# Optimization experiments

Measured on AMD Instinct MI355X. Metric: run time of the kernel, lower is better.

## Reference

```python
import jax, jax.numpy as jnp
import numpy as np
from jax import lax

RADIUS = 4
SIGMA_1 = 5.0
SIGMA_2 = 1.0


def _gaussian_kernel_3d(radius, sigma):
    x = np.linspace(-radius, radius, 2 * radius + 1)
    xx, yy, zz = np.meshgrid(x, x, x)
    dist2 = xx ** 2 + yy ** 2 + zz ** 2
    k = np.exp(-dist2 / (2.0 * sigma ** 2)).astype(np.float32)
    return jnp.asarray(k)[None, None]  # [O=1, I=1, D, H, W]


def _conv3d_same(x, kernel, radius):
    # x: [B,1,D,H,W], kernel: [1,1,kd,kh,kw]
    pad = [(radius, radius)] * 3
    return lax.conv_general_dilated(
        x, kernel, window_strides=(1, 1, 1), padding=pad,
        dimension_numbers=('NCDHW', 'OIDHW', 'NCDHW'))


def setup_inputs() -> dict:
    key = jax.random.key(0)
    k1, k2 = jax.random.split(key)
    labels = jax.random.uniform(k1, (4, 1, 160, 160, 160), dtype=jnp.float32)
    inputs = jax.random.uniform(k2, (4, 1, 160, 160, 160), dtype=jnp.float32)
    return {"labels": labels, "inputs": inputs}


def reference(labels, inputs):
    kernel = _gaussian_kernel_3d(RADIUS, SIGMA_1)
    num_classes = 2
    p0 = labels[:, 0:1]  # [B,1,D,H,W]
    loss = jnp.float32(0.0)
    for k in range(num_classes):
        class_probs = p0 if k == 0 else 1.0 - p0
        class_mean = (jnp.mean(inputs * class_probs, axis=(2, 3, 4), keepdims=True)
                      / (jnp.mean(class_probs, axis=(2, 3, 4), keepdims=True) + 1e-5))
        diff = jnp.sum((inputs - class_mean) ** 2, axis=1, keepdims=True)  # [B,1,D,H,W]
        weights = jnp.exp(-(diff ** 2) / (SIGMA_2 ** 2))
        numerator = jnp.sum(class_probs * _conv3d_same(class_probs * weights, kernel, RADIUS))
        denominator = jnp.sum(class_probs * _conv3d_same(weights, kernel, RADIUS))
        # L1Loss(scalar, 0) == abs(scalar)
        loss = loss + jnp.abs(numerator / (denominator + 1e-6))
    return jnp.float32(num_classes) - loss
```

## Files before the change

### kernel.cpp

```cpp
#include <hip/hip_runtime.h>
#include <math.h>

#define NX   160
#define N2   25600
#define N3   4096000
#define NB   4

#define NTILES_XY 16000
#define TILES_PER_B 4000
#define NBLK_Z 800

#define SA_W 52
#define SB_W 36

__device__ __constant__ float G1[9] = {
    0.72614903f, 0.83527021f, 0.92311635f, 0.98019867f, 1.0f,
    0.98019867f, 0.92311635f, 0.83527021f, 0.72614903f};

#define ES_FULL 7.92946852f
__device__ __constant__ float ES_M[4] = {3.46473426f, 2.48453559f, 1.56141924f,
                                         0.72614903f};
__device__ inline float edge_sum(int i) {
    float s = ES_FULL;
    if (i < 4) s -= ES_M[i];
    if (i > NX - 5) s -= ES_M[NX - 1 - i];
    return s;
}

__device__ inline float4 f4_zero() { return make_float4(0.f, 0.f, 0.f, 0.f); }
__device__ inline float4 f4_axpy(float a, float4 b, float4 c) {
    return make_float4(c.x + a * b.x, c.y + a * b.y, c.z + a * b.z, c.w + a * b.w);
}

template <int NV>
__device__ inline void block_reduce_store(double* vals, double* dst) {
    __shared__ double red[4][NV];
    int lane = threadIdx.x & 63;
    int wave = threadIdx.x >> 6;
#pragma unroll
    for (int v = 0; v < NV; ++v) {
        double x = vals[v];
#pragma unroll
        for (int off = 32; off > 0; off >>= 1) x += __shfl_down(x, off, 64);
        if (lane == 0) red[wave][v] = x;
    }
    __syncthreads();
    if (threadIdx.x < NV) {
        int v = threadIdx.x;
        dst[v] = red[0][v] + red[1][v] + red[2][v] + red[3][v];
    }
}

__global__ __launch_bounds__(256) void conv_xy_kernel(
    const float* __restrict__ labels, const float* __restrict__ inputs,
    float* __restrict__ t, double* __restrict__ pS) {
    __shared__ float sA[40 * SA_W];
    __shared__ float sB[40 * SB_W];

    int bid = blockIdx.x;
    int tileX = bid % 5;
    int tileY = (bid / 5) % 5;
    int zb = bid / 25;
    int sliceOff = zb * N2;
    int x0 = tileX * 32, y0 = tileY * 32;
    int tid = threadIdx.x;

    for (int i = tid; i < 480; i += 256) {
        int row = i / 12, c = i % 12;
        int gx = x0 - 8 + 4 * c;
        int gy = y0 - 4 + row;
        float4 v = f4_zero();
        if (gy >= 0 && gy < NX && gx >= 0 && gx <= NX - 4)
            v = *(const float4*)&labels[sliceOff + gy * NX + gx];
        *(float4*)&sA[row * SA_W + 4 * c] = v;
    }
    __syncthreads();

    for (int i = tid; i < 320; i += 256) {
        int r = i >> 3, x4 = i & 7;
        const float* row = &sA[r * SA_W + 4 * x4];
        float4 a = *(const float4*)&row[4];
        float4 b = *(const float4*)&row[8];
        float4 c = *(const float4*)&row[12];
        float w[12] = {a.x, a.y, a.z, a.w, b.x, b.y, b.z, b.w,
                       c.x, c.y, c.z, c.w};
        float4 o = f4_zero();
#pragma unroll
        for (int d = 0; d < 9; ++d) {
            float g = G1[d];
            o.x += g * w[d];
            o.y += g * w[d + 1];
            o.z += g * w[d + 2];
            o.w += g * w[d + 3];
        }
        *(float4*)&sB[r * SB_W + 4 * x4] = o;
    }
    __syncthreads();

    int oy = tid >> 3, x4 = tid & 7;
    float4 acc = f4_zero();
#pragma unroll
    for (int d = 0; d < 9; ++d) {
        float4 v = *(const float4*)&sB[(oy + d) * SB_W + 4 * x4];
        acc = f4_axpy(G1[d], v, acc);
    }
    int gi = sliceOff + (y0 + oy) * NX + (x0 + 4 * x4);
    *(float4*)&t[gi] = acc;

    float4 p = *(const float4*)&sA[(oy + 4) * SA_W + 4 * x4 + 8];
    float4 in = *(const float4*)&inputs[gi];
    float sp = p.x + p.y + p.z + p.w;
    float sip = in.x * p.x + in.y * p.y + in.z * p.z + in.w * p.w;
    float si = in.x + in.y + in.z + in.w;
    double vals[3] = {(double)sp, (double)sip, (double)si};
    block_reduce_store<3>(vals, pS + 3 * bid);
}

__global__ __launch_bounds__(256) void reduce_S_kernel(
    const double* __restrict__ pS, double* __restrict__ S) {
    int b = blockIdx.x;
    double v0 = 0, v1 = 0, v2 = 0;
    for (int i = threadIdx.x; i < TILES_PER_B; i += 256) {
        const double* p = pS + 3 * (b * TILES_PER_B + i);
        v0 += p[0]; v1 += p[1]; v2 += p[2];
    }
    double vals[3] = {v0, v1, v2};
    block_reduce_store<3>(vals, S + 3 * b);
}

__global__ __launch_bounds__(256) void conv_z_reduce_kernel(
    const float* __restrict__ t, const float* __restrict__ labels,
    const float* __restrict__ inputs, const double* __restrict__ S,
    double* __restrict__ pZ) {
    int tidg = blockIdx.x * 256 + threadIdx.x;
    int x4 = tidg % 40;
    int r = tidg / 40;
    int y = r % NX;
    r /= NX;
    int zc = r % 8;
    int b = r / 8;

    double sp = S[3 * b + 0], sip = S[3 * b + 1], si = S[3 * b + 2];
    const double Nv = (double)N3;
    float m0 = (float)((sip / Nv) / (sp / Nv + 1e-5));
    float m1 = (float)(((si - sip) / Nv) / ((Nv - sp) / Nv + 1e-5));

    int x = x4 * 4;
    float ey = edge_sum(y);
    float cx[4] = {edge_sum(x) * ey, edge_sum(x + 1) * ey,
                   edge_sum(x + 2) * ey, edge_sum(x + 3) * ey};

    int z0 = zc * 20;
    int base = b * N3 + y * NX + x;

    float4 win[9];
#pragma unroll
    for (int d = 0; d < 9; ++d) {
        int z = z0 - 4 + d;
        win[d] = (z >= 0 && z < NX) ? *(const float4*)&t[base + z * N2]
                                    : f4_zero();
    }

    float n0 = 0.f, d0 = 0.f, n1 = 0.f, d1 = 0.f;
    for (int zb = 0; zb < 5; ++zb) {
        int z = z0 + 4 * zb;
        float4 tn[4], pv[4], iv[4];
#pragma unroll
        for (int j = 0; j < 4; ++j) {
            int zl = z + j + 5;
            tn[j] = (zl < NX) ? *(const float4*)&t[base + zl * N2] : f4_zero();
            int gi = base + (z + j) * N2;
            pv[j] = *(const float4*)&labels[gi];
            iv[j] = *(const float4*)&inputs[gi];
        }
#pragma unroll
        for (int j = 0; j < 4; ++j) {
            float4 c4 = f4_zero();
#pragma unroll
            for (int d = 0; d < 9; ++d) c4 = f4_axpy(G1[d], win[d], c4);
            float ez = edge_sum(z + j);
            float pc[4] = {pv[j].x, pv[j].y, pv[j].z, pv[j].w};
            float ic[4] = {iv[j].x, iv[j].y, iv[j].z, iv[j].w};
            float cc[4] = {c4.x, c4.y, c4.z, c4.w};
#pragma unroll
            for (int l = 0; l < 4; ++l) {
                float c1 = cx[l] * ez - cc[l];
                float df0 = ic[l] - m0; df0 *= df0;
                float w0 = __expf(-df0 * df0);
                float df1 = ic[l] - m1; df1 *= df1;
                float w1 = __expf(-df1 * df1);
                n0 += cc[l] * pc[l] * w0;
                d0 += cc[l] * w0;
                n1 += c1 * (1.f - pc[l]) * w1;
                d1 += c1 * w1;
            }
#pragma unroll
            for (int d = 0; d < 8; ++d) win[d] = win[d + 1];
            win[8] = tn[j];
        }
    }
    double vals[4] = {(double)n0, (double)d0, (double)n1, (double)d1};
    block_reduce_store<4>(vals, pZ + 4 * blockIdx.x);
}

__global__ __launch_bounds__(256) void finalize_kernel(
    const double* __restrict__ pZ, float* __restrict__ out) {
    double a0 = 0, a1 = 0, a2 = 0, a3 = 0;
    for (int i = threadIdx.x; i < NBLK_Z; i += 256) {
        const double* p = pZ + 4 * i;
        a0 += p[0]; a1 += p[1]; a2 += p[2]; a3 += p[3];
    }
    __shared__ double red[4][4];
    int lane = threadIdx.x & 63;
    int wave = threadIdx.x >> 6;
    double vals[4] = {a0, a1, a2, a3};
#pragma unroll
    for (int v = 0; v < 4; ++v) {
        double x = vals[v];
#pragma unroll
        for (int off = 32; off > 0; off >>= 1) x += __shfl_down(x, off, 64);
        if (lane == 0) red[wave][v] = x;
    }
    __syncthreads();
    if (threadIdx.x == 0) {
        double acc[4];
#pragma unroll
        for (int v = 0; v < 4; ++v)
            acc[v] = red[0][v] + red[1][v] + red[2][v] + red[3][v];
        double r0 = fabs(acc[0] / (acc[1] + 1e-6));
        double r1 = fabs(acc[2] / (acc[3] + 1e-6));
        out[0] = (float)(2.0 - r0 - r1);
    }
}

extern "C" void kernel_launch(void* const* d_in, const int* in_sizes, int n_in,
                              void* d_out, int out_size, void* d_ws, size_t ws_size,
                              hipStream_t stream) {
    const float* labels = (const float*)d_in[0];
    const float* inputs = (const float*)d_in[1];
    float* out = (float*)d_out;

    double* pS = (double*)d_ws;
    double* S  = (double*)((char*)d_ws + 384000);
    double* pZ = (double*)((char*)d_ws + 384096);
    float*  t  = (float*)((char*)d_ws + 524288);

    hipLaunchKernelGGL(conv_xy_kernel, dim3(NTILES_XY), dim3(256), 0, stream,
                       labels, inputs, t, pS);
    hipLaunchKernelGGL(reduce_S_kernel, dim3(NB), dim3(256), 0, stream, pS, S);
    hipLaunchKernelGGL(conv_z_reduce_kernel, dim3(NBLK_Z), dim3(256), 0, stream,
                       t, labels, inputs, S, pZ);
    hipLaunchKernelGGL(finalize_kernel, dim3(1), dim3(256), 0, stream, pZ, out);
}
```

Measured before the change: 206.4 us.

## Fuse XY and Z convolution passes per slab, dropping intermediate volume

Removes the global intermediate XY-convolved volume. Each block now recomputes the XY convolution of labels plane by plane in shared memory and streams the results through a 9-deep Z register window over a 10-plane slab. Global sums move into a separate streaming reduction kernel. This avoids writing and re-reading a 65MB intermediate, at the cost of recomputing 8 halo planes per slab (about 1.8x XY work) and many more syncthreads.

```diff
diff --git a/kernel.cpp b/kernel.cpp
--- a/kernel.cpp
+++ b/kernel.cpp
@@ -6,9 +6,10 @@
 #define N3   4096000
 #define NB   4
 
-#define NTILES_XY 16000
-#define TILES_PER_B 4000
-#define NBLK_Z 800
+#define Z_SLAB 10
+#define NBLK_F 1600
+#define NBLK_S 1000
+#define SBLK_PER_B 250
 
 #define SA_W 52
 #define SB_W 36
@@ -51,34 +52,23 @@
     }
 }
 
-__global__ __launch_bounds__(256) void conv_xy_kernel(
-    const float* __restrict__ labels, const float* __restrict__ inputs,
-    float* __restrict__ t, double* __restrict__ pS) {
-    __shared__ float sA[40 * SA_W];
-    __shared__ float sB[40 * SB_W];
-
-    int bid = blockIdx.x;
-    int tileX = bid % 5;
-    int tileY = (bid / 5) % 5;
-    int zb = bid / 25;
-    int sliceOff = zb * N2;
-    int x0 = tileX * 32, y0 = tileY * 32;
-    int tid = threadIdx.x;
-
+__device__ inline float4 t_plane(const float* __restrict__ labels,
+                                 float* sA, float* sB, int planeOff,
+                                 int x0, int y0, int tid, int oy, int x4) {
     for (int i = tid; i < 480; i += 256) {
         int row = i / 12, c = i % 12;
         int gx = x0 - 8 + 4 * c;
         int gy = y0 - 4 + row;
         float4 v = f4_zero();
         if (gy >= 0 && gy < NX && gx >= 0 && gx <= NX - 4)
-            v = *(const float4*)&labels[sliceOff + gy * NX + gx];
+            v = *(const float4*)&labels[planeOff + gy * NX + gx];
         *(float4*)&sA[row * SA_W + 4 * c] = v;
     }
     __syncthreads();
 
     for (int i = tid; i < 320; i += 256) {
-        int r = i >> 3, x4 = i & 7;
-        const float* row = &sA[r * SA_W + 4 * x4];
+        int r = i >> 3, xx = i & 7;
+        const float* row = &sA[r * SA_W + 4 * xx];
         float4 a = *(const float4*)&row[4];
         float4 b = *(const float4*)&row[8];
         float4 c = *(const float4*)&row[12];
@@ -93,25 +83,37 @@
             o.z += g * w[d + 2];
             o.w += g * w[d + 3];
         }
-        *(float4*)&sB[r * SB_W + 4 * x4] = o;
-    }
-    __syncthreads();
-
-    int oy = tid >> 3, x4 = tid & 7;
+        *(float4*)&sB[r * SB_W + 4 * xx] = o;
+    }
+    __syncthreads();
+
     float4 acc = f4_zero();
 #pragma unroll
     for (int d = 0; d < 9; ++d) {
         float4 v = *(const float4*)&sB[(oy + d) * SB_W + 4 * x4];
         acc = f4_axpy(G1[d], v, acc);
     }
-    int gi = sliceOff + (y0 + oy) * NX + (x0 + 4 * x4);
-    *(float4*)&t[gi] = acc;
-
-    float4 p = *(const float4*)&sA[(oy + 4) * SA_W + 4 * x4 + 8];
-    float4 in = *(const float4*)&inputs[gi];
-    float sp = p.x + p.y + p.z + p.w;
-    float sip = in.x * p.x + in.y * p.y + in.z * p.z + in.w * p.w;
-    float si = in.x + in.y + in.z + in.w;
+    return acc;
+}
+
+__global__ __launch_bounds__(256) void sums_kernel(
+    const float* __restrict__ labels, const float* __restrict__ inputs,
+    double* __restrict__ pS) {
+    int bid = blockIdx.x, tid = threadIdx.x;
+    int b = bid / SBLK_PER_B;
+    int blk = bid % SBLK_PER_B;
+    int base = b * N3;
+    float sp = 0.f, sip = 0.f, si = 0.f;
+#pragma unroll 4
+    for (int k = 0; k < 16; ++k) {
+        int f4i = blk * 256 + tid + k * 64000;
+        int gi = base + 4 * f4i;
+        float4 p = *(const float4*)&labels[gi];
+        float4 in = *(const float4*)&inputs[gi];
+        sp += p.x + p.y + p.z + p.w;
+        sip += in.x * p.x + in.y * p.y + in.z * p.z + in.w * p.w;
+        si += in.x + in.y + in.z + in.w;
+    }
     double vals[3] = {(double)sp, (double)sip, (double)si};
     block_reduce_store<3>(vals, pS + 3 * bid);
 }
@@ -120,94 +122,95 @@
     const double* __restrict__ pS, double* __restrict__ S) {
     int b = blockIdx.x;
     double v0 = 0, v1 = 0, v2 = 0;
-    for (int i = threadIdx.x; i < TILES_PER_B; i += 256) {
-        const double* p = pS + 3 * (b * TILES_PER_B + i);
+    for (int i = threadIdx.x; i < SBLK_PER_B; i += 256) {
+        const double* p = pS + 3 * (b * SBLK_PER_B + i);
         v0 += p[0]; v1 += p[1]; v2 += p[2];
     }
     double vals[3] = {v0, v1, v2};
     block_reduce_store<3>(vals, S + 3 * b);
 }
 
-__global__ __launch_bounds__(256) void conv_z_reduce_kernel(
-    const float* __restrict__ t, const float* __restrict__ labels,
-    const float* __restrict__ inputs, const double* __restrict__ S,
-    double* __restrict__ pZ) {
-    int tidg = blockIdx.x * 256 + threadIdx.x;
-    int x4 = tidg % 40;
-    int r = tidg / 40;
-    int y = r % NX;
-    r /= NX;
-    int zc = r % 8;
-    int b = r / 8;
+__global__ __launch_bounds__(256) void fused_xyz_kernel(
+    const float* __restrict__ labels, const float* __restrict__ inputs,
+    const double* __restrict__ S, double* __restrict__ pZ) {
+    __shared__ float sA[40 * SA_W];
+    __shared__ float sB[40 * SB_W];
+
+    int tid = threadIdx.x;
+    int bid = blockIdx.x;
+    int tileX = bid % 5;
+    int tileY = (bid / 5) % 5;
+    int slab = (bid / 25) % 16;
+    int b = bid / 400;
+    int x0 = tileX * 32, y0 = tileY * 32, z0 = slab * Z_SLAB;
+    int oy = tid >> 3, x4 = tid & 7;
+    int volBase = b * N3;
 
     double sp = S[3 * b + 0], sip = S[3 * b + 1], si = S[3 * b + 2];
     const double Nv = (double)N3;
     float m0 = (float)((sip / Nv) / (sp / Nv + 1e-5));
     float m1 = (float)(((si - sip) / Nv) / ((Nv - sp) / Nv + 1e-5));
 
-    int x = x4 * 4;
-    float ey = edge_sum(y);
-    float cx[4] = {edge_sum(x) * ey, edge_sum(x + 1) * ey,
-                   edge_sum(x + 2) * ey, edge_sum(x + 3) * ey};
-
-    int z0 = zc * 20;
-    int base = b * N3 + y * NX + x;
+    int gx = x0 + 4 * x4;
+    float ey = edge_sum(y0 + oy);
+    float cx[4] = {edge_sum(gx) * ey, edge_sum(gx + 1) * ey,
+                   edge_sum(gx + 2) * ey, edge_sum(gx + 3) * ey};
+    int ctr = volBase + (y0 + oy) * NX + gx;
 
     float4 win[9];
 #pragma unroll
     for (int d = 0; d < 9; ++d) {
         int z = z0 - 4 + d;
-        win[d] = (z >= 0 && z < NX) ? *(const float4*)&t[base + z * N2]
-                                    : f4_zero();
+        win[d] = (z >= 0 && z < NX)
+                     ? t_plane(labels, sA, sB, volBase + z * N2, x0, y0, tid, oy, x4)
+                     : f4_zero();
     }
 
     float n0 = 0.f, d0 = 0.f, n1 = 0.f, d1 = 0.f;
-    for (int zb = 0; zb < 5; ++zb) {
-        int z = z0 + 4 * zb;
-        float4 tn[4], pv[4], iv[4];
-#pragma unroll
-        for (int j = 0; j < 4; ++j) {
-            int zl = z + j + 5;
-            tn[j] = (zl < NX) ? *(const float4*)&t[base + zl * N2] : f4_zero();
-            int gi = base + (z + j) * N2;
-            pv[j] = *(const float4*)&labels[gi];
-            iv[j] = *(const float4*)&inputs[gi];
+    for (int j = 0; j < Z_SLAB; ++j) {
+        int z = z0 + j;
+        float4 c4 = f4_zero();
+#pragma unroll
+        for (int d = 0; d < 9; ++d) c4 = f4_axpy(G1[d], win[d], c4);
+
+        float4 pv = *(const float4*)&labels[ctr + z * N2];
+        float4 iv = *(const float4*)&inputs[ctr + z * N2];
+        float ez = edge_sum(z);
+        float pc[4] = {pv.x, pv.y, pv.z, pv.w};
+        float ic[4] = {iv.x, iv.y, iv.z, iv.w};
+        float cc[4] = {c4.x, c4.y, c4.z, c4.w};
+#pragma unroll
+        for (int l = 0; l < 4; ++l) {
+            float c1 = cx[l] * ez - cc[l];
+            float df0 = ic[l] - m0; df0 *= df0;
+            float w0 = __expf(-df0 * df0);
+            float df1 = ic[l] - m1; df1 *= df1;
+            float w1 = __expf(-df1 * df1);
+            n0 += cc[l] * pc[l] * w0;
+            d0 += cc[l] * w0;
+            n1 += c1 * (1.f - pc[l]) * w1;
+            d1 += c1 * w1;
         }
-#pragma unroll
-        for (int j = 0; j < 4; ++j) {
-            float4 c4 = f4_zero();
-#pragma unroll
-            for (int d = 0; d < 9; ++d) c4 = f4_axpy(G1[d], win[d], c4);
-            float ez = edge_sum(z + j);
-            float pc[4] = {pv[j].x, pv[j].y, pv[j].z, pv[j].w};
-            float ic[4] = {iv[j].x, iv[j].y, iv[j].z, iv[j].w};
-            float cc[4] = {c4.x, c4.y, c4.z, c4.w};
-#pragma unroll
-            for (int l = 0; l < 4; ++l) {
-                float c1 = cx[l] * ez - cc[l];
-                float df0 = ic[l] - m0; df0 *= df0;
-                float w0 = __expf(-df0 * df0);
-                float df1 = ic[l] - m1; df1 *= df1;
-                float w1 = __expf(-df1 * df1);
-                n0 += cc[l] * pc[l] * w0;
-                d0 += cc[l] * w0;
-                n1 += c1 * (1.f - pc[l]) * w1;
-                d1 += c1 * w1;
-            }
+
+        if (j < Z_SLAB - 1) {
+            int zn = z0 + j + 5;
+            float4 nw = (zn < NX)
+                            ? t_plane(labels, sA, sB, volBase + zn * N2, x0, y0, tid, oy, x4)
+                            : f4_zero();
 #pragma unroll
             for (int d = 0; d < 8; ++d) win[d] = win[d + 1];
-            win[8] = tn[j];
+            win[8] = nw;
         }
     }
     double vals[4] = {(double)n0, (double)d0, (double)n1, (double)d1};
-    block_reduce_store<4>(vals, pZ + 4 * blockIdx.x);
+    block_reduce_store<4>(vals, pZ + 4 * bid);
 }
 
 __global__ __launch_bounds__(256) void finalize_kernel(
     const double* __restrict__ pZ, float* __restrict__ out) {
     double a0 = 0, a1 = 0, a2 = 0, a3 = 0;
-    for (int i = threadIdx.x; i < NBLK_Z; i += 256) {
-        const double* p = pZ + 4 * i;
+    for (int i = threadIdx.x; i < NBLK_F; i += 256) {
+        const double* p = &pZ[4 * i];
         a0 += p[0]; a1 += p[1]; a2 += p[2]; a3 += p[3];
     }
     __shared__ double red[4][4];
@@ -241,14 +244,13 @@
     float* out = (float*)d_out;
 
     double* pS = (double*)d_ws;
-    double* S  = (double*)((char*)d_ws + 384000);
-    double* pZ = (double*)((char*)d_ws + 384096);
-    float*  t  = (float*)((char*)d_ws + 524288);
-
-    hipLaunchKernelGGL(conv_xy_kernel, dim3(NTILES_XY), dim3(256), 0, stream,
-                       labels, inputs, t, pS);
+    double* S  = (double*)((char*)d_ws + 24064);
+    double* pZ = (double*)((char*)d_ws + 24320);
+
+    hipLaunchKernelGGL(sums_kernel, dim3(NBLK_S), dim3(256), 0, stream,
+                       labels, inputs, pS);
     hipLaunchKernelGGL(reduce_S_kernel, dim3(NB), dim3(256), 0, stream, pS, S);
-    hipLaunchKernelGGL(conv_z_reduce_kernel, dim3(NBLK_Z), dim3(256), 0, stream,
-                       t, labels, inputs, S, pZ);
+    hipLaunchKernelGGL(fused_xyz_kernel, dim3(NBLK_F), dim3(256), 0, stream,
+                       labels, inputs, S, pZ);
     hipLaunchKernelGGL(finalize_kernel, dim3(1), dim3(256), 0, stream, pZ, out);
 }
```

New measurement: 244.9 us. +18.6%, slower.
